# Optimization experiments

Measured on AMD Instinct MI355X. Metric: run time of the kernel, lower is better.

The kernel has to match this reference:

```python
import jax, jax.numpy as jnp
import numpy as np

HEADS = 16
EMBED = 1024


def setup_inputs() -> dict:
    key = jax.random.key(0)
    k1, k2, k3, k4, k5, k6 = jax.random.split(key, 6)
    N, S, E = 2, 2048, EMBED
    return {
        "values": jax.random.normal(k1, (N, S, E), dtype=jnp.float32),
        "keys": jax.random.normal(k2, (N, S, E), dtype=jnp.float32),
        "query": jax.random.normal(k3, (N, S, E), dtype=jnp.float32),
        "mask": jax.random.randint(k4, (N, 1, S, S), 0, 2, dtype=jnp.int32),
        "W_out": jax.random.normal(k5, (E, E), dtype=jnp.float32) * 0.02,
        "b_out": jax.random.normal(k6, (E,), dtype=jnp.float32) * 0.02,
    }


def reference(values, keys, query, mask, W_out, b_out):
    N, Q, E = query.shape
    K = keys.shape[1]
    H = HEADS
    D = E // H
    v = values.reshape(N, K, H, D)
    k = keys.reshape(N, K, H, D)
    q = query.reshape(N, Q, H, D)
    # [N, H, Q, K] score matrix (faithful to the naive einsum formulation)
    energy = jnp.einsum("nqhd,nkhd->nhqk", q, k)
    energy = jnp.where(mask == 0, jnp.float32(-1e20), energy)
    # NOTE: original scales by sqrt(embed_size), not sqrt(head_dim)
    attention = jax.nn.softmax(energy / jnp.sqrt(jnp.float32(E)), axis=3)
    out = jnp.einsum("nhqk,nkhd->nqhd", attention, v).reshape(N, Q, E)
    return out @ W_out.T + b_out
```

## Files before the change

kernel.cpp:

```cpp
#include <hip/hip_runtime.h>
#include <hip/hip_bf16.h>


#define S_LEN  2048
#define EMB    1024
#define NHEAD  16
#define DHEAD  64
#define NBATCH 2

#define KSC 0.04508422002778011f

typedef float              f32x4    __attribute__((ext_vector_type(4)));
typedef float              f32x16   __attribute__((ext_vector_type(16)));
typedef __bf16             bf16x8   __attribute__((ext_vector_type(8)));
typedef unsigned short     ushort8v __attribute__((ext_vector_type(8)));
typedef unsigned long long u64;

union FragU { ushort8v u; bf16x8 b; };
union BFrag { unsigned u32[4]; bf16x8 b; };

__device__ __forceinline__ unsigned short f2b(float f) {
  union { __hip_bfloat16 h; unsigned short u; } c;
  c.h = __float2bfloat16(f);
  return c.u;
}

__device__ __forceinline__ unsigned int cvt_pk_bf16(float lo, float hi) {
  unsigned int r;
  asm("v_cvt_pk_bf16_f32 %0, %1, %2" : "=v"(r) : "v"(lo), "v"(hi));
  return r;
}

#define PSWAP(a, b) asm("v_permlane32_swap_b32 %0, %1" : "+v"(a), "+v"(b))

#define GLD16(g, l)                                                            \
  __builtin_amdgcn_global_load_lds(                                            \
      (__attribute__((address_space(1))) void*)(g),                            \
      (__attribute__((address_space(3))) void*)(l), 16, 0, 0)

__global__ __launch_bounds__(256) void prep(
    const float* __restrict__ Wo, unsigned short* __restrict__ Wb,
    const float* __restrict__ Kg, unsigned short* __restrict__ Kb,
    const float* __restrict__ Vg, unsigned short* __restrict__ Vt,
    const int* __restrict__ Mg,   u64* __restrict__ Mb)
{
  const int bid = blockIdx.x;
  const int tid = threadIdx.x;
  if (bid < 2560) {
    const float* X = (bid < 512) ? Wo : Kg;
    unsigned short* Y = (bid < 512) ? Wb : Kb;
    const int bb = (bid < 512) ? bid : bid - 512;
    const size_t i = ((size_t)bb * 256 + tid) * 8;
    float4 a = *reinterpret_cast<const float4*>(X + i);
    float4 b = *reinterpret_cast<const float4*>(X + i + 4);
    ushort8v u;
    u[0] = f2b(a.x); u[1] = f2b(a.y); u[2] = f2b(a.z); u[3] = f2b(a.w);
    u[4] = f2b(b.x); u[5] = f2b(b.y); u[6] = f2b(b.z); u[7] = f2b(b.w);
    *reinterpret_cast<ushort8v*>(Y + i) = u;
  } else if (bid < 3584) {
    __shared__ unsigned short T[64][72];
    const int b2 = bid - 2560;
    const int sb = b2 & 31, h = (b2 >> 5) & 15, n = b2 >> 9;
    const int r = tid >> 2, cb = (tid & 3) * 16;
    const float* src = Vg + ((size_t)(n * S_LEN + sb * 64 + r)) * EMB + h * DHEAD + cb;
    ushort8v u0, u1;
#pragma unroll
    for (int j = 0; j < 2; ++j) {
      float4 x = *reinterpret_cast<const float4*>(src + j * 4);
      u0[j*4+0] = f2b(x.x); u0[j*4+1] = f2b(x.y); u0[j*4+2] = f2b(x.z); u0[j*4+3] = f2b(x.w);
      float4 y = *reinterpret_cast<const float4*>(src + 8 + j * 4);
      u1[j*4+0] = f2b(y.x); u1[j*4+1] = f2b(y.y); u1[j*4+2] = f2b(y.z); u1[j*4+3] = f2b(y.w);
    }
    *reinterpret_cast<ushort8v*>(&T[r][cb])     = u0;
    *reinterpret_cast<ushort8v*>(&T[r][cb + 8]) = u1;
    __syncthreads();
    const int d = tid >> 2, sc_ = (tid & 3) * 16;
    ushort8v o0, o1;
#pragma unroll
    for (int j = 0; j < 8; ++j) { o0[j] = T[sc_ + j][d]; o1[j] = T[sc_ + 8 + j][d]; }
    unsigned short* dst = Vt + ((size_t)((n * NHEAD + h) * DHEAD + d)) * S_LEN + sb * 64 + sc_;
    *reinterpret_cast<ushort8v*>(dst)     = o0;
    *reinterpret_cast<ushort8v*>(dst + 8) = o1;
  } else {
    const int b3 = bid - 3584;
    const size_t base = (size_t)b3 * 1024 + (tid >> 6) * 256;
    const int l = tid & 63;
#pragma unroll
    for (int j = 0; j < 4; ++j) {
      const int v = Mg[base + j * 64 + l];
      u64 bj = __ballot(v != 0);
      if (l == 0) Mb[base / 64 + j] = bj;
    }
  }
}

__global__ __launch_bounds__(512, 4) void attn_fwd(
    const unsigned short* __restrict__ Kb,
    const unsigned short* __restrict__ Vtg,
    const float* __restrict__ Qg,
    const u64* __restrict__ Mbit,
    unsigned short* __restrict__ Og)
{
  __shared__ __attribute__((aligned(16))) char SMEM[65536];

  const int bid = blockIdx.x;
  const int qb = bid & 15, h = (bid >> 4) & 15, n = bid >> 8;
  const int nh = n * NHEAD + h;
  const int tid = threadIdx.x;
  const int w = tid >> 6, sp = w >> 2, wq = w & 3;
  const int l = tid & 63, q5 = l & 31, hi = l >> 5;
  const int hi4 = hi * 4;
  const int q0w = qb * 128 + wq * 32;
  const int qg = q0w + q5;

  FragU qf[4];
  {
    const float* qp = Qg + ((size_t)(n * S_LEN + qg)) * EMB + h * DHEAD + hi * 8;
#pragma unroll
    for (int s = 0; s < 4; ++s) {
      float4 a = *reinterpret_cast<const float4*>(qp + s * 16);
      float4 b = *reinterpret_cast<const float4*>(qp + s * 16 + 4);
      ushort8v u;
      u[0] = f2b(a.x * KSC); u[1] = f2b(a.y * KSC); u[2] = f2b(a.z * KSC); u[3] = f2b(a.w * KSC);
      u[4] = f2b(b.x * KSC); u[5] = f2b(b.y * KSC); u[6] = f2b(b.z * KSC); u[7] = f2b(b.w * KSC);
      qf[s].u = u;
    }
  }

  FragU ones;
#pragma unroll
  for (int j = 0; j < 8; ++j) ones.u[j] = 0x3F80;

  f32x16 acc0 = {}, acc1 = {}, racc = {};

  const int t8 = tid & 255;
  const int srow = t8 >> 3, sc = t8 & 7;
  const char* kbase = (const char*)Kb +
      ((size_t)(n * S_LEN + sp * 1024 + srow)) * 2048 + h * 128 +
      ((sc * 16) ^ ((srow & 7) << 4));
  const char* vbase = (const char*)Vtg +
      ((size_t)(nh * DHEAD + srow)) * 4096 + sp * 2048 +
      ((sc * 16) ^ ((srow & 7) << 4));

  char* Ksp = SMEM + sp * 16384;
  char* Vsp = SMEM + 32768 + sp * 16384;
  const int fsw = (l & 7) << 4;

  const u64* Mq = Mbit + ((size_t)(n * S_LEN + qg)) * 32 + sp * 16;
  u64 mq_cur = Mq[0];

#define ATTN_STAGE(BUF, IT) do {                                               \
    GLD16(kbase + (size_t)(IT) * 131072,          Ksp + (BUF) * 8192 + t8 * 16); \
    GLD16(kbase + (size_t)(IT) * 131072 + 65536,  Ksp + (BUF) * 8192 + 4096 + t8 * 16); \
    GLD16(vbase + (size_t)(IT) * 128,             Vsp + (BUF) * 8192 + t8 * 16); \
    GLD16(vbase + (size_t)(IT) * 128 + 131072,    Vsp + (BUF) * 8192 + 4096 + t8 * 16); \
  } while (0)

#define ATTN_TILE(BUF, IT) do {                                                \
    __syncthreads();                                                           \
    if ((IT) + 1 < 16) ATTN_STAGE((BUF) ^ 1, (IT) + 1);                        \
    const u64 mrow_ = mq_cur;                                                  \
    if ((IT) + 1 < 16) mq_cur = Mq[(IT) + 1];                                  \
    _Pragma("unroll") for (int b = 0; b < 2; ++b) {                            \
      f32x16 Sb = {};                                                          \
      __builtin_amdgcn_s_setprio(1);                                           \
      _Pragma("unroll") for (int s = 0; s < 4; ++s) {                          \
        FragU kf_;                                                             \
        kf_.u = *reinterpret_cast<const ushort8v*>(                            \
            Ksp + (BUF) * 8192 + ((b * 32 + q5) * 128 + ((s * 32 + hi * 16) ^ fsw))); \
        Sb = __builtin_amdgcn_mfma_f32_32x32x16_bf16(kf_.b, qf[s].b, Sb, 0, 0, 0); \
      }                                                                        \
      __builtin_amdgcn_s_setprio(0);                                           \
      const unsigned m32_ = b ? (unsigned)(mrow_ >> 32) : (unsigned)mrow_;     \
      float p_[16];                                                            \
      _Pragma("unroll") for (int t = 0; t < 4; ++t) {                          \
        const unsigned nib_ = m32_ >> (8 * t + hi4);                           \
        _Pragma("unroll") for (int e = 0; e < 4; ++e) {                        \
          const int r = 4 * t + e;                                             \
          float ex_ = __builtin_amdgcn_exp2f(Sb[r]);                           \
          const unsigned sm_ = (unsigned)((int)(nib_ << (31 - e)) >> 31);      \
          p_[r] = __uint_as_float(__float_as_uint(ex_) & sm_);                 \
        }                                                                      \
      }                                                                        \
      unsigned U0 = cvt_pk_bf16(p_[0],  p_[1]),  U1 = cvt_pk_bf16(p_[2],  p_[3]); \
      unsigned U2 = cvt_pk_bf16(p_[4],  p_[5]),  U3 = cvt_pk_bf16(p_[6],  p_[7]); \
      unsigned U4 = cvt_pk_bf16(p_[8],  p_[9]),  U5 = cvt_pk_bf16(p_[10], p_[11]); \
      unsigned U6 = cvt_pk_bf16(p_[12], p_[13]), U7 = cvt_pk_bf16(p_[14], p_[15]); \
      PSWAP(U0, U2); PSWAP(U1, U3); PSWAP(U4, U6); PSWAP(U5, U7);              \
      BFrag F0, F1;                                                            \
      F0.u32[0] = U0; F0.u32[1] = U1; F0.u32[2] = U2; F0.u32[3] = U3;          \
      F1.u32[0] = U4; F1.u32[1] = U5; F1.u32[2] = U6; F1.u32[3] = U7;          \
      __builtin_amdgcn_s_setprio(1);                                           \
      racc = __builtin_amdgcn_mfma_f32_32x32x16_bf16(ones.b, F0.b, racc, 0, 0, 0); \
      racc = __builtin_amdgcn_mfma_f32_32x32x16_bf16(ones.b, F1.b, racc, 0, 0, 0); \
      _Pragma("unroll") for (int db = 0; db < 2; ++db) {                       \
        FragU vf0_, vf1_;                                                      \
        vf0_.u = *reinterpret_cast<const ushort8v*>(                           \
            Vsp + (BUF) * 8192 + ((db * 32 + q5) * 128 + (((2 * b) * 32 + hi * 16) ^ fsw))); \
        vf1_.u = *reinterpret_cast<const ushort8v*>(                           \
            Vsp + (BUF) * 8192 + ((db * 32 + q5) * 128 + (((2 * b + 1) * 32 + hi * 16) ^ fsw))); \
        if (db == 0) {                                                         \
          acc0 = __builtin_amdgcn_mfma_f32_32x32x16_bf16(vf0_.b, F0.b, acc0, 0, 0, 0); \
          acc0 = __builtin_amdgcn_mfma_f32_32x32x16_bf16(vf1_.b, F1.b, acc0, 0, 0, 0); \
        } else {                                                               \
          acc1 = __builtin_amdgcn_mfma_f32_32x32x16_bf16(vf0_.b, F0.b, acc1, 0, 0, 0); \
          acc1 = __builtin_amdgcn_mfma_f32_32x32x16_bf16(vf1_.b, F1.b, acc1, 0, 0, 0); \
        }                                                                      \
      }                                                                        \
      __builtin_amdgcn_s_setprio(0);                                           \
    }                                                                          \
  } while (0)

  ATTN_STAGE(0, 0);
  for (int it = 0; it < 16; it += 2) {
    ATTN_TILE(0, it);
    ATTN_TILE(1, it + 1);
  }

  const float rs = racc[0];
  const int esw = (l & 7) << 4;

  __syncthreads();
  if (sp == 1) {
#pragma unroll
    for (int i = 0; i < 4; ++i) {
      f32x4 v0 = (f32x4){acc0[4*i], acc0[4*i+1], acc0[4*i+2], acc0[4*i+3]};
      f32x4 v1 = (f32x4){acc1[4*i], acc1[4*i+1], acc1[4*i+2], acc1[4*i+3]};
      *reinterpret_cast<f32x4*>(SMEM + wq * 8192 + l * 128 + ((i * 16) ^ esw))      = v0;
      *reinterpret_cast<f32x4*>(SMEM + wq * 8192 + l * 128 + ((64 + i * 16) ^ esw)) = v1;
    }
    *reinterpret_cast<float*>(SMEM + 32768 + wq * 256 + l * 4) = rs;
  }
  __syncthreads();
  if (sp == 0) {
    const float ors = *reinterpret_cast<const float*>(SMEM + 32768 + wq * 256 + l * 4);
    const float rin = 1.0f / (rs + ors);
    unsigned short* orow = Og + ((size_t)(n * S_LEN + qg)) * EMB + h * DHEAD + hi4;
#pragma unroll
    for (int db = 0; db < 2; ++db) {
#pragma unroll
      for (int t = 0; t < 4; ++t) {
        f32x4 pa = *reinterpret_cast<const f32x4*>(
            SMEM + wq * 8192 + l * 128 + ((db * 64 + t * 16) ^ esw));
        float a0, a1, a2, a3;
        if (db == 0) {
          a0 = (acc0[4*t]   + pa[0]) * rin; a1 = (acc0[4*t+1] + pa[1]) * rin;
          a2 = (acc0[4*t+2] + pa[2]) * rin; a3 = (acc0[4*t+3] + pa[3]) * rin;
        } else {
          a0 = (acc1[4*t]   + pa[0]) * rin; a1 = (acc1[4*t+1] + pa[1]) * rin;
          a2 = (acc1[4*t+2] + pa[2]) * rin; a3 = (acc1[4*t+3] + pa[3]) * rin;
        }
        uint2 pk;
        pk.x = cvt_pk_bf16(a0, a1);
        pk.y = cvt_pk_bf16(a2, a3);
        *reinterpret_cast<uint2*>(orow + db * 32 + t * 8) = pk;
      }
    }
  }
}

__global__ __launch_bounds__(256) void out_proj(
    const unsigned short* __restrict__ A,
    const unsigned short* __restrict__ W,
    const float* __restrict__ bias,
    float* __restrict__ Y)
{
  __shared__ __attribute__((aligned(16))) unsigned short At[2][8192];
  __shared__ __attribute__((aligned(16))) unsigned short Bt[2][4096];

  const int bid = blockIdx.x;
  const int nb = bid & 15, mb = bid >> 4;
  const int tid = threadIdx.x;
  const int w = tid >> 6, l = tid & 63, lg = l >> 4, li = l & 15;
  const int m0 = mb * 128, n0 = nb * 64;

  f32x4 acc[2][4];
#pragma unroll
  for (int g = 0; g < 2; ++g)
#pragma unroll
    for (int c = 0; c < 4; ++c) acc[g][c] = (f32x4){0.f, 0.f, 0.f, 0.f};

  const int srow8  = tid >> 3;
  const int schunk = (tid & 7) * 16;
  const int ssw    = (srow8 & 7) << 4;
  const char* abase = (const char*)A + ((size_t)m0 + srow8) * (EMB * 2) + (schunk ^ ssw);
  const char* bbase = (const char*)W + ((size_t)n0 + srow8) * (EMB * 2) + (schunk ^ ssw);
  const int rsw = (li & 7) << 4;

#define PROJ_STAGE(BUF, KK) do {                                               \
    const char* ab_ = abase + (KK) * 128;                                      \
    const char* bb_ = bbase + (KK) * 128;                                      \
    GLD16(ab_,             (char*)At + (BUF) * 16384 + w * 1024);              \
    GLD16(ab_ + 32 * 2048, (char*)At + (BUF) * 16384 + 4096 + w * 1024);       \
    GLD16(ab_ + 64 * 2048, (char*)At + (BUF) * 16384 + 8192 + w * 1024);       \
    GLD16(ab_ + 96 * 2048, (char*)At + (BUF) * 16384 + 12288 + w * 1024);      \
    GLD16(bb_,             (char*)Bt + (BUF) * 8192 + w * 1024);               \
    GLD16(bb_ + 32 * 2048, (char*)Bt + (BUF) * 8192 + 4096 + w * 1024);        \
  } while (0)

#define PROJ_TILE(BUF, KK) do {                                                \
    __syncthreads();                                                           \
    if ((KK) + 1 < 16) PROJ_STAGE((BUF) ^ 1, (KK) + 1);                        \
    __builtin_amdgcn_s_setprio(1);                                             \
    _Pragma("unroll") for (int s = 0; s < 2; ++s) {                            \
      FragU af_[2];                                                            \
      _Pragma("unroll") for (int g = 0; g < 2; ++g)                            \
        af_[g].u = *reinterpret_cast<const ushort8v*>(                         \
            (char*)At + (BUF) * 16384 +                                        \
            ((w * 32 + g * 16 + li) * 128 + ((s * 64 + lg * 16) ^ rsw)));      \
      _Pragma("unroll") for (int c = 0; c < 4; ++c) {                          \
        FragU bf_;                                                             \
        bf_.u = *reinterpret_cast<const ushort8v*>(                            \
            (char*)Bt + (BUF) * 8192 +                                         \
            ((c * 16 + li) * 128 + ((s * 64 + lg * 16) ^ rsw)));               \
        acc[0][c] = __builtin_amdgcn_mfma_f32_16x16x32_bf16(af_[0].b, bf_.b, acc[0][c], 0, 0, 0); \
        acc[1][c] = __builtin_amdgcn_mfma_f32_16x16x32_bf16(af_[1].b, bf_.b, acc[1][c], 0, 0, 0); \
      }                                                                        \
    }                                                                          \
    __builtin_amdgcn_s_setprio(0);                                             \
  } while (0)

  PROJ_STAGE(0, 0);
  for (int kk = 0; kk < 16; kk += 2) {
    PROJ_TILE(0, kk);
    PROJ_TILE(1, kk + 1);
  }

#pragma unroll
  for (int g = 0; g < 2; ++g)
#pragma unroll
    for (int c = 0; c < 4; ++c) {
      const float bv = bias[n0 + c * 16 + li];
#pragma unroll
      for (int r = 0; r < 4; ++r) {
        const int row = m0 + w * 32 + g * 16 + lg * 4 + r;
        Y[(size_t)row * EMB + n0 + c * 16 + li] = acc[g][c][r] + bv;
      }
    }
}

extern "C" void kernel_launch(void* const* d_in, const int* in_sizes, int n_in,
                              void* d_out, int out_size, void* d_ws, size_t ws_size,
                              hipStream_t stream) {
  const float* Vg = (const float*)d_in[0];
  const float* Kg = (const float*)d_in[1];
  const float* Qg = (const float*)d_in[2];
  const int*   Mg = (const int*)d_in[3];
  const float* Wo = (const float*)d_in[4];
  const float* bo = (const float*)d_in[5];
  float* Y = (float*)d_out;

  char* ws = (char*)d_ws;
  unsigned short* Og   = (unsigned short*)(ws);
  unsigned short* Wb   = (unsigned short*)(ws + (8u << 20));
  unsigned short* Kb16 = (unsigned short*)(ws + (10u << 20));
  unsigned short* Vt   = (unsigned short*)(ws + (18u << 20));
  u64*            Mbit = (u64*)(ws + (26u << 20));

  hipLaunchKernelGGL(prep, dim3(11776), dim3(256), 0, stream,
                     Wo, Wb, Kg, Kb16, Vg, Vt, Mg, Mbit);
  hipLaunchKernelGGL(attn_fwd, dim3(NBATCH * NHEAD * (S_LEN / 128)), dim3(512), 0, stream,
                     Kb16, Vt, Qg, Mbit, Og);
  hipLaunchKernelGGL(out_proj, dim3((NBATCH * S_LEN / 128) * (EMB / 64)), dim3(256), 0, stream,
                     Og, Wb, bo, Y);
}
```

Before: 88.92 us.

## Drop LDS staging in attention, load K/V fragments directly from global memory

The attention kernel drops its LDS double-buffered K/V staging and the two-way key split with its cross-warp reduction. Each of four warps now reads K and V fragments straight from global memory (relying on L2) for all 32 key tiles. Q is pre-converted to scaled bf16 in the prep kernel, and blocks are remapped so neighbouring blocks share heads. This removes barriers and LDS traffic but adds redundant global loads per warp, exposes load latency with no explicit prefetch, and cuts threads per block.

```diff
diff --git a/kernel.cpp b/kernel.cpp
--- a/kernel.cpp
+++ b/kernel.cpp
@@ -41,25 +41,27 @@
 __global__ __launch_bounds__(256) void prep(
     const float* __restrict__ Wo, unsigned short* __restrict__ Wb,
     const float* __restrict__ Kg, unsigned short* __restrict__ Kb,
+    const float* __restrict__ Qg, unsigned short* __restrict__ Qb,
     const float* __restrict__ Vg, unsigned short* __restrict__ Vt,
     const int* __restrict__ Mg,   u64* __restrict__ Mb)
 {
   const int bid = blockIdx.x;
   const int tid = threadIdx.x;
-  if (bid < 2560) {
-    const float* X = (bid < 512) ? Wo : Kg;
-    unsigned short* Y = (bid < 512) ? Wb : Kb;
-    const int bb = (bid < 512) ? bid : bid - 512;
+  if (bid < 4608) {
+    const float* X; unsigned short* Y; int bb; float scl;
+    if (bid < 512)       { X = Wo; Y = Wb; bb = bid;        scl = 1.f; }
+    else if (bid < 2560) { X = Kg; Y = Kb; bb = bid - 512;  scl = 1.f; }
+    else                 { X = Qg; Y = Qb; bb = bid - 2560; scl = KSC; }
     const size_t i = ((size_t)bb * 256 + tid) * 8;
     float4 a = *reinterpret_cast<const float4*>(X + i);
     float4 b = *reinterpret_cast<const float4*>(X + i + 4);
     ushort8v u;
-    u[0] = f2b(a.x); u[1] = f2b(a.y); u[2] = f2b(a.z); u[3] = f2b(a.w);
-    u[4] = f2b(b.x); u[5] = f2b(b.y); u[6] = f2b(b.z); u[7] = f2b(b.w);
+    u[0] = f2b(a.x * scl); u[1] = f2b(a.y * scl); u[2] = f2b(a.z * scl); u[3] = f2b(a.w * scl);
+    u[4] = f2b(b.x * scl); u[5] = f2b(b.y * scl); u[6] = f2b(b.z * scl); u[7] = f2b(b.w * scl);
     *reinterpret_cast<ushort8v*>(Y + i) = u;
-  } else if (bid < 3584) {
+  } else if (bid < 5632) {
     __shared__ unsigned short T[64][72];
-    const int b2 = bid - 2560;
+    const int b2 = bid - 4608;
     const int sb = b2 & 31, h = (b2 >> 5) & 15, n = b2 >> 9;
     const int r = tid >> 2, cb = (tid & 3) * 16;
     const float* src = Vg + ((size_t)(n * S_LEN + sb * 64 + r)) * EMB + h * DHEAD + cb;
@@ -82,7 +84,7 @@
     *reinterpret_cast<ushort8v*>(dst)     = o0;
     *reinterpret_cast<ushort8v*>(dst + 8) = o1;
   } else {
-    const int b3 = bid - 3584;
+    const int b3 = bid - 5632;
     const size_t base = (size_t)b3 * 1024 + (tid >> 6) * 256;
     const int l = tid & 63;
 #pragma unroll
@@ -94,37 +96,29 @@
   }
 }
 
-__global__ __launch_bounds__(512, 4) void attn_fwd(
+__global__ __launch_bounds__(256, 4) void attn_fwd(
     const unsigned short* __restrict__ Kb,
     const unsigned short* __restrict__ Vtg,
-    const float* __restrict__ Qg,
+    const unsigned short* __restrict__ Qb,
     const u64* __restrict__ Mbit,
     unsigned short* __restrict__ Og)
 {
-  __shared__ __attribute__((aligned(16))) char SMEM[65536];
-
-  const int bid = blockIdx.x;
-  const int qb = bid & 15, h = (bid >> 4) & 15, n = bid >> 8;
+  const int bid0 = blockIdx.x;
+  const int ob = ((bid0 & 7) << 6) | (bid0 >> 3);
+  const int qb = ob & 15, h = (ob >> 4) & 15, n = ob >> 8;
   const int nh = n * NHEAD + h;
   const int tid = threadIdx.x;
-  const int w = tid >> 6, sp = w >> 2, wq = w & 3;
+  const int w = tid >> 6;
   const int l = tid & 63, q5 = l & 31, hi = l >> 5;
   const int hi4 = hi * 4;
-  const int q0w = qb * 128 + wq * 32;
-  const int qg = q0w + q5;
+  const int qg = qb * 128 + w * 32 + q5;
 
   FragU qf[4];
   {
-    const float* qp = Qg + ((size_t)(n * S_LEN + qg)) * EMB + h * DHEAD + hi * 8;
-#pragma unroll
-    for (int s = 0; s < 4; ++s) {
-      float4 a = *reinterpret_cast<const float4*>(qp + s * 16);
-      float4 b = *reinterpret_cast<const float4*>(qp + s * 16 + 4);
-      ushort8v u;
-      u[0] = f2b(a.x * KSC); u[1] = f2b(a.y * KSC); u[2] = f2b(a.z * KSC); u[3] = f2b(a.w * KSC);
-      u[4] = f2b(b.x * KSC); u[5] = f2b(b.y * KSC); u[6] = f2b(b.z * KSC); u[7] = f2b(b.w * KSC);
-      qf[s].u = u;
-    }
+    const unsigned short* qp = Qb + ((size_t)(n * S_LEN + qg)) * EMB + h * DHEAD + hi * 8;
+#pragma unroll
+    for (int s = 0; s < 4; ++s)
+      qf[s].u = *reinterpret_cast<const ushort8v*>(qp + s * 16);
   }
 
   FragU ones;
@@ -133,128 +127,81 @@
 
   f32x16 acc0 = {}, acc1 = {}, racc = {};
 
-  const int t8 = tid & 255;
-  const int srow = t8 >> 3, sc = t8 & 7;
-  const char* kbase = (const char*)Kb +
-      ((size_t)(n * S_LEN + sp * 1024 + srow)) * 2048 + h * 128 +
-      ((sc * 16) ^ ((srow & 7) << 4));
-  const char* vbase = (const char*)Vtg +
-      ((size_t)(nh * DHEAD + srow)) * 4096 + sp * 2048 +
-      ((sc * 16) ^ ((srow & 7) << 4));
-
-  char* Ksp = SMEM + sp * 16384;
-  char* Vsp = SMEM + 32768 + sp * 16384;
-  const int fsw = (l & 7) << 4;
-
-  const u64* Mq = Mbit + ((size_t)(n * S_LEN + qg)) * 32 + sp * 16;
-  u64 mq_cur = Mq[0];
-
-#define ATTN_STAGE(BUF, IT) do {                                               \
-    GLD16(kbase + (size_t)(IT) * 131072,          Ksp + (BUF) * 8192 + t8 * 16); \
-    GLD16(kbase + (size_t)(IT) * 131072 + 65536,  Ksp + (BUF) * 8192 + 4096 + t8 * 16); \
-    GLD16(vbase + (size_t)(IT) * 128,             Vsp + (BUF) * 8192 + t8 * 16); \
-    GLD16(vbase + (size_t)(IT) * 128 + 131072,    Vsp + (BUF) * 8192 + 4096 + t8 * 16); \
-  } while (0)
-
-#define ATTN_TILE(BUF, IT) do {                                                \
-    __syncthreads();                                                           \
-    if ((IT) + 1 < 16) ATTN_STAGE((BUF) ^ 1, (IT) + 1);                        \
-    const u64 mrow_ = mq_cur;                                                  \
-    if ((IT) + 1 < 16) mq_cur = Mq[(IT) + 1];                                  \
-    _Pragma("unroll") for (int b = 0; b < 2; ++b) {                            \
-      f32x16 Sb = {};                                                          \
-      __builtin_amdgcn_s_setprio(1);                                           \
-      _Pragma("unroll") for (int s = 0; s < 4; ++s) {                          \
-        FragU kf_;                                                             \
-        kf_.u = *reinterpret_cast<const ushort8v*>(                            \
-            Ksp + (BUF) * 8192 + ((b * 32 + q5) * 128 + ((s * 32 + hi * 16) ^ fsw))); \
-        Sb = __builtin_amdgcn_mfma_f32_32x32x16_bf16(kf_.b, qf[s].b, Sb, 0, 0, 0); \
-      }                                                                        \
-      __builtin_amdgcn_s_setprio(0);                                           \
-      const unsigned m32_ = b ? (unsigned)(mrow_ >> 32) : (unsigned)mrow_;     \
-      float p_[16];                                                            \
-      _Pragma("unroll") for (int t = 0; t < 4; ++t) {                          \
-        const unsigned nib_ = m32_ >> (8 * t + hi4);                           \
-        _Pragma("unroll") for (int e = 0; e < 4; ++e) {                        \
-          const int r = 4 * t + e;                                             \
-          float ex_ = __builtin_amdgcn_exp2f(Sb[r]);                           \
-          const unsigned sm_ = (unsigned)((int)(nib_ << (31 - e)) >> 31);      \
-          p_[r] = __uint_as_float(__float_as_uint(ex_) & sm_);                 \
-        }                                                                      \
-      }                                                                        \
-      unsigned U0 = cvt_pk_bf16(p_[0],  p_[1]),  U1 = cvt_pk_bf16(p_[2],  p_[3]); \
-      unsigned U2 = cvt_pk_bf16(p_[4],  p_[5]),  U3 = cvt_pk_bf16(p_[6],  p_[7]); \
-      unsigned U4 = cvt_pk_bf16(p_[8],  p_[9]),  U5 = cvt_pk_bf16(p_[10], p_[11]); \
-      unsigned U6 = cvt_pk_bf16(p_[12], p_[13]), U7 = cvt_pk_bf16(p_[14], p_[15]); \
-      PSWAP(U0, U2); PSWAP(U1, U3); PSWAP(U4, U6); PSWAP(U5, U7);              \
-      BFrag F0, F1;                                                            \
-      F0.u32[0] = U0; F0.u32[1] = U1; F0.u32[2] = U2; F0.u32[3] = U3;          \
-      F1.u32[0] = U4; F1.u32[1] = U5; F1.u32[2] = U6; F1.u32[3] = U7;          \
-      __builtin_amdgcn_s_setprio(1);                                           \
-      racc = __builtin_amdgcn_mfma_f32_32x32x16_bf16(ones.b, F0.b, racc, 0, 0, 0); \
-      racc = __builtin_amdgcn_mfma_f32_32x32x16_bf16(ones.b, F1.b, racc, 0, 0, 0); \
-      _Pragma("unroll") for (int db = 0; db < 2; ++db) {                       \
-        FragU vf0_, vf1_;                                                      \
-        vf0_.u = *reinterpret_cast<const ushort8v*>(                           \
-            Vsp + (BUF) * 8192 + ((db * 32 + q5) * 128 + (((2 * b) * 32 + hi * 16) ^ fsw))); \
-        vf1_.u = *reinterpret_cast<const ushort8v*>(                           \
-            Vsp + (BUF) * 8192 + ((db * 32 + q5) * 128 + (((2 * b + 1) * 32 + hi * 16) ^ fsw))); \
-        if (db == 0) {                                                         \
-          acc0 = __builtin_amdgcn_mfma_f32_32x32x16_bf16(vf0_.b, F0.b, acc0, 0, 0, 0); \
-          acc0 = __builtin_amdgcn_mfma_f32_32x32x16_bf16(vf1_.b, F1.b, acc0, 0, 0, 0); \
-        } else {                                                               \
-          acc1 = __builtin_amdgcn_mfma_f32_32x32x16_bf16(vf0_.b, F0.b, acc1, 0, 0, 0); \
-          acc1 = __builtin_amdgcn_mfma_f32_32x32x16_bf16(vf1_.b, F1.b, acc1, 0, 0, 0); \
-        }                                                                      \
-      }                                                                        \
-      __builtin_amdgcn_s_setprio(0);                                           \
-    }                                                                          \
-  } while (0)
-
-  ATTN_STAGE(0, 0);
-  for (int it = 0; it < 16; it += 2) {
-    ATTN_TILE(0, it);
-    ATTN_TILE(1, it + 1);
-  }
-
-  const float rs = racc[0];
-  const int esw = (l & 7) << 4;
-
-  __syncthreads();
-  if (sp == 1) {
-#pragma unroll
-    for (int i = 0; i < 4; ++i) {
-      f32x4 v0 = (f32x4){acc0[4*i], acc0[4*i+1], acc0[4*i+2], acc0[4*i+3]};
-      f32x4 v1 = (f32x4){acc1[4*i], acc1[4*i+1], acc1[4*i+2], acc1[4*i+3]};
-      *reinterpret_cast<f32x4*>(SMEM + wq * 8192 + l * 128 + ((i * 16) ^ esw))      = v0;
-      *reinterpret_cast<f32x4*>(SMEM + wq * 8192 + l * 128 + ((64 + i * 16) ^ esw)) = v1;
-    }
-    *reinterpret_cast<float*>(SMEM + 32768 + wq * 256 + l * 4) = rs;
-  }
-  __syncthreads();
-  if (sp == 0) {
-    const float ors = *reinterpret_cast<const float*>(SMEM + 32768 + wq * 256 + l * 4);
-    const float rin = 1.0f / (rs + ors);
-    unsigned short* orow = Og + ((size_t)(n * S_LEN + qg)) * EMB + h * DHEAD + hi4;
-#pragma unroll
-    for (int db = 0; db < 2; ++db) {
+  const char* kbl = (const char*)Kb + ((size_t)(n * S_LEN) + q5) * 2048 + h * 128 + hi * 16;
+  const char* vbl = (const char*)Vtg + ((size_t)(nh * DHEAD) + q5) * 4096 + hi * 16;
+  const u64* Mq = Mbit + ((size_t)(n * S_LEN) + qg) * 32;
+
+#pragma unroll 2
+  for (int it = 0; it < 32; ++it) {
+    const u64 mrow = Mq[it];
+    const char* kt = kbl + (size_t)it * 131072;
+    const char* vt = vbl + (size_t)it * 128;
+#pragma unroll
+    for (int b = 0; b < 2; ++b) {
+      f32x16 Sb = {};
+#pragma unroll
+      for (int s = 0; s < 4; ++s) {
+        FragU kf;
+        kf.u = *reinterpret_cast<const ushort8v*>(kt + b * 65536 + s * 32);
+        Sb = __builtin_amdgcn_mfma_f32_32x32x16_bf16(kf.b, qf[s].b, Sb, 0, 0, 0);
+      }
+      const unsigned m32_ = b ? (unsigned)(mrow >> 32) : (unsigned)mrow;
+      float p_[16];
 #pragma unroll
       for (int t = 0; t < 4; ++t) {
-        f32x4 pa = *reinterpret_cast<const f32x4*>(
-            SMEM + wq * 8192 + l * 128 + ((db * 64 + t * 16) ^ esw));
-        float a0, a1, a2, a3;
+        const unsigned nib_ = m32_ >> (8 * t + hi4);
+#pragma unroll
+        for (int e = 0; e < 4; ++e) {
+          const int r = 4 * t + e;
+          float ex_ = __builtin_amdgcn_exp2f(Sb[r]);
+          const unsigned sm_ = (unsigned)((int)(nib_ << (31 - e)) >> 31);
+          p_[r] = __uint_as_float(__float_as_uint(ex_) & sm_);
+        }
+      }
+      unsigned U0 = cvt_pk_bf16(p_[0],  p_[1]),  U1 = cvt_pk_bf16(p_[2],  p_[3]);
+      unsigned U2 = cvt_pk_bf16(p_[4],  p_[5]),  U3 = cvt_pk_bf16(p_[6],  p_[7]);
+      unsigned U4 = cvt_pk_bf16(p_[8],  p_[9]),  U5 = cvt_pk_bf16(p_[10], p_[11]);
+      unsigned U6 = cvt_pk_bf16(p_[12], p_[13]), U7 = cvt_pk_bf16(p_[14], p_[15]);
+      PSWAP(U0, U2); PSWAP(U1, U3); PSWAP(U4, U6); PSWAP(U5, U7);
+      BFrag F0, F1;
+      F0.u32[0] = U0; F0.u32[1] = U1; F0.u32[2] = U2; F0.u32[3] = U3;
+      F1.u32[0] = U4; F1.u32[1] = U5; F1.u32[2] = U6; F1.u32[3] = U7;
+      racc = __builtin_amdgcn_mfma_f32_32x32x16_bf16(ones.b, F0.b, racc, 0, 0, 0);
+      racc = __builtin_amdgcn_mfma_f32_32x32x16_bf16(ones.b, F1.b, racc, 0, 0, 0);
+#pragma unroll
+      for (int db = 0; db < 2; ++db) {
+        FragU vf0, vf1;
+        vf0.u = *reinterpret_cast<const ushort8v*>(vt + db * 131072 + (2 * b) * 32);
+        vf1.u = *reinterpret_cast<const ushort8v*>(vt + db * 131072 + (2 * b + 1) * 32);
         if (db == 0) {
-          a0 = (acc0[4*t]   + pa[0]) * rin; a1 = (acc0[4*t+1] + pa[1]) * rin;
-          a2 = (acc0[4*t+2] + pa[2]) * rin; a3 = (acc0[4*t+3] + pa[3]) * rin;
+          acc0 = __builtin_amdgcn_mfma_f32_32x32x16_bf16(vf0.b, F0.b, acc0, 0, 0, 0);
+          acc0 = __builtin_amdgcn_mfma_f32_32x32x16_bf16(vf1.b, F1.b, acc0, 0, 0, 0);
         } else {
-          a0 = (acc1[4*t]   + pa[0]) * rin; a1 = (acc1[4*t+1] + pa[1]) * rin;
-          a2 = (acc1[4*t+2] + pa[2]) * rin; a3 = (acc1[4*t+3] + pa[3]) * rin;
+          acc1 = __builtin_amdgcn_mfma_f32_32x32x16_bf16(vf0.b, F0.b, acc1, 0, 0, 0);
+          acc1 = __builtin_amdgcn_mfma_f32_32x32x16_bf16(vf1.b, F1.b, acc1, 0, 0, 0);
         }
-        uint2 pk;
-        pk.x = cvt_pk_bf16(a0, a1);
-        pk.y = cvt_pk_bf16(a2, a3);
-        *reinterpret_cast<uint2*>(orow + db * 32 + t * 8) = pk;
-      }
+      }
+    }
+  }
+
+  const float rin = 1.0f / racc[0];
+  unsigned short* orow = Og + ((size_t)(n * S_LEN + qg)) * EMB + h * DHEAD + hi4;
+#pragma unroll
+  for (int db = 0; db < 2; ++db) {
+#pragma unroll
+    for (int t = 0; t < 4; ++t) {
+      float a0, a1, a2, a3;
+      if (db == 0) {
+        a0 = acc0[4*t] * rin;   a1 = acc0[4*t+1] * rin;
+        a2 = acc0[4*t+2] * rin; a3 = acc0[4*t+3] * rin;
+      } else {
+        a0 = acc1[4*t] * rin;   a1 = acc1[4*t+1] * rin;
+        a2 = acc1[4*t+2] * rin; a3 = acc1[4*t+3] * rin;
+      }
+      uint2 pk;
+      pk.x = cvt_pk_bf16(a0, a1);
+      pk.y = cvt_pk_bf16(a2, a3);
+      *reinterpret_cast<uint2*>(orow + db * 32 + t * 8) = pk;
     }
   }
 }
@@ -356,11 +303,12 @@
   unsigned short* Kb16 = (unsigned short*)(ws + (10u << 20));
   unsigned short* Vt   = (unsigned short*)(ws + (18u << 20));
   u64*            Mbit = (u64*)(ws + (26u << 20));
-
-  hipLaunchKernelGGL(prep, dim3(11776), dim3(256), 0, stream,
-                     Wo, Wb, Kg, Kb16, Vg, Vt, Mg, Mbit);
-  hipLaunchKernelGGL(attn_fwd, dim3(NBATCH * NHEAD * (S_LEN / 128)), dim3(512), 0, stream,
-                     Kb16, Vt, Qg, Mbit, Og);
+  unsigned short* Qb16 = (unsigned short*)(ws + (27u << 20));
+
+  hipLaunchKernelGGL(prep, dim3(13824), dim3(256), 0, stream,
+                     Wo, Wb, Kg, Kb16, Qg, Qb16, Vg, Vt, Mg, Mbit);
+  hipLaunchKernelGGL(attn_fwd, dim3(NBATCH * NHEAD * (S_LEN / 128)), dim3(256), 0, stream,
+                     Kb16, Vt, Qb16, Mbit, Og);
   hipLaunchKernelGGL(out_proj, dim3((NBATCH * S_LEN / 128) * (EMB / 64)), dim3(256), 0, stream,
                      Og, Wb, bo, Y);
 }
```

Result: slower. 170.8 us (+92.1%).

## Enlarge out_proj tile to 128x128 with 2x2 warp layout

Applied to the files above, without the earlier changes.

The output projection GEMM now uses 128x128 output tiles instead of 128x64. Each of the four waves computes a 64x64 subtile with 4x4 MFMA accumulators, which raises operand reuse from LDS and halves the number of workgroups to 256. LDS staging is merged into one 64KB buffer, setprio hints are removed, and launch bounds request two blocks per CU. The cost is higher register pressure and fewer blocks to fill the GPU, which leaves some CUs idle on a 256-CU device.

```diff
diff --git a/kernel.cpp b/kernel.cpp
--- a/kernel.cpp
+++ b/kernel.cpp
@@ -259,65 +259,64 @@
   }
 }
 
-__global__ __launch_bounds__(256) void out_proj(
+__global__ __launch_bounds__(256, 2) void out_proj(
     const unsigned short* __restrict__ A,
     const unsigned short* __restrict__ W,
     const float* __restrict__ bias,
     float* __restrict__ Y)
 {
-  __shared__ __attribute__((aligned(16))) unsigned short At[2][8192];
-  __shared__ __attribute__((aligned(16))) unsigned short Bt[2][4096];
+  __shared__ __attribute__((aligned(16))) char PSM[65536];
 
   const int bid = blockIdx.x;
-  const int nb = bid & 15, mb = bid >> 4;
+  const int nb = bid & 7, mb = bid >> 3;
   const int tid = threadIdx.x;
-  const int w = tid >> 6, l = tid & 63, lg = l >> 4, li = l & 15;
-  const int m0 = mb * 128, n0 = nb * 64;
-
-  f32x4 acc[2][4];
-#pragma unroll
-  for (int g = 0; g < 2; ++g)
-#pragma unroll
-    for (int c = 0; c < 4; ++c) acc[g][c] = (f32x4){0.f, 0.f, 0.f, 0.f};
-
-  const int srow8  = tid >> 3;
-  const int schunk = (tid & 7) * 16;
-  const int ssw    = (srow8 & 7) << 4;
-  const char* abase = (const char*)A + ((size_t)m0 + srow8) * (EMB * 2) + (schunk ^ ssw);
-  const char* bbase = (const char*)W + ((size_t)n0 + srow8) * (EMB * 2) + (schunk ^ ssw);
+  const int w = tid >> 6, wr = w >> 1, wc = w & 1;
+  const int l = tid & 63, lg = l >> 4, li = l & 15;
+  const int m0 = mb * 128, n0 = nb * 128;
+
+  f32x4 acc[4][4];
+#pragma unroll
+  for (int mi = 0; mi < 4; ++mi)
+#pragma unroll
+    for (int ci = 0; ci < 4; ++ci) acc[mi][ci] = (f32x4){0.f, 0.f, 0.f, 0.f};
+
+  const int srow = tid >> 3;
+  const int sch  = (tid & 7) * 16;
+  const int ssw  = (srow & 7) << 4;
+  const char* abase = (const char*)A + ((size_t)(m0 + srow)) * 2048 + (sch ^ ssw);
+  const char* bbase = (const char*)W + ((size_t)(n0 + srow)) * 2048 + (sch ^ ssw);
   const int rsw = (li & 7) << 4;
 
+  char* Asm = PSM;
+  char* Bsm = PSM + 32768;
+
 #define PROJ_STAGE(BUF, KK) do {                                               \
-    const char* ab_ = abase + (KK) * 128;                                      \
-    const char* bb_ = bbase + (KK) * 128;                                      \
-    GLD16(ab_,             (char*)At + (BUF) * 16384 + w * 1024);              \
-    GLD16(ab_ + 32 * 2048, (char*)At + (BUF) * 16384 + 4096 + w * 1024);       \
-    GLD16(ab_ + 64 * 2048, (char*)At + (BUF) * 16384 + 8192 + w * 1024);       \
-    GLD16(ab_ + 96 * 2048, (char*)At + (BUF) * 16384 + 12288 + w * 1024);      \
-    GLD16(bb_,             (char*)Bt + (BUF) * 8192 + w * 1024);               \
-    GLD16(bb_ + 32 * 2048, (char*)Bt + (BUF) * 8192 + 4096 + w * 1024);        \
+    _Pragma("unroll") for (int j = 0; j < 4; ++j) {                            \
+      GLD16(abase + (size_t)j * 65536 + (KK) * 128,                            \
+            Asm + (BUF) * 16384 + j * 4096 + tid * 16);                        \
+      GLD16(bbase + (size_t)j * 65536 + (KK) * 128,                            \
+            Bsm + (BUF) * 16384 + j * 4096 + tid * 16);                        \
+    }                                                                          \
   } while (0)
 
 #define PROJ_TILE(BUF, KK) do {                                                \
     __syncthreads();                                                           \
     if ((KK) + 1 < 16) PROJ_STAGE((BUF) ^ 1, (KK) + 1);                        \
-    __builtin_amdgcn_s_setprio(1);                                             \
     _Pragma("unroll") for (int s = 0; s < 2; ++s) {                            \
-      FragU af_[2];                                                            \
-      _Pragma("unroll") for (int g = 0; g < 2; ++g)                            \
-        af_[g].u = *reinterpret_cast<const ushort8v*>(                         \
-            (char*)At + (BUF) * 16384 +                                        \
-            ((w * 32 + g * 16 + li) * 128 + ((s * 64 + lg * 16) ^ rsw)));      \
-      _Pragma("unroll") for (int c = 0; c < 4; ++c) {                          \
-        FragU bf_;                                                             \
-        bf_.u = *reinterpret_cast<const ushort8v*>(                            \
-            (char*)Bt + (BUF) * 8192 +                                         \
-            ((c * 16 + li) * 128 + ((s * 64 + lg * 16) ^ rsw)));               \
-        acc[0][c] = __builtin_amdgcn_mfma_f32_16x16x32_bf16(af_[0].b, bf_.b, acc[0][c], 0, 0, 0); \
-        acc[1][c] = __builtin_amdgcn_mfma_f32_16x16x32_bf16(af_[1].b, bf_.b, acc[1][c], 0, 0, 0); \
-      }                                                                        \
+      FragU af_[4], bf_[4];                                                    \
+      _Pragma("unroll") for (int mi = 0; mi < 4; ++mi)                         \
+        af_[mi].u = *reinterpret_cast<const ushort8v*>(                        \
+            Asm + (BUF) * 16384 +                                              \
+            ((wr * 64 + mi * 16 + li) * 128 + ((s * 64 + lg * 16) ^ rsw)));    \
+      _Pragma("unroll") for (int ci = 0; ci < 4; ++ci)                         \
+        bf_[ci].u = *reinterpret_cast<const ushort8v*>(                        \
+            Bsm + (BUF) * 16384 +                                              \
+            ((wc * 64 + ci * 16 + li) * 128 + ((s * 64 + lg * 16) ^ rsw)));    \
+      _Pragma("unroll") for (int mi = 0; mi < 4; ++mi)                         \
+        _Pragma("unroll") for (int ci = 0; ci < 4; ++ci)                       \
+          acc[mi][ci] = __builtin_amdgcn_mfma_f32_16x16x32_bf16(               \
+              af_[mi].b, bf_[ci].b, acc[mi][ci], 0, 0, 0);                     \
     }                                                                          \
-    __builtin_amdgcn_s_setprio(0);                                             \
   } while (0)
 
   PROJ_STAGE(0, 0);
@@ -327,16 +326,18 @@
   }
 
 #pragma unroll
-  for (int g = 0; g < 2; ++g)
-#pragma unroll
-    for (int c = 0; c < 4; ++c) {
-      const float bv = bias[n0 + c * 16 + li];
+  for (int ci = 0; ci < 4; ++ci) {
+    const int col = n0 + wc * 64 + ci * 16 + li;
+    const float bv = bias[col];
+#pragma unroll
+    for (int mi = 0; mi < 4; ++mi) {
 #pragma unroll
       for (int r = 0; r < 4; ++r) {
-        const int row = m0 + w * 32 + g * 16 + lg * 4 + r;
-        Y[(size_t)row * EMB + n0 + c * 16 + li] = acc[g][c][r] + bv;
+        const int row = m0 + wr * 64 + mi * 16 + lg * 4 + r;
+        Y[(size_t)row * EMB + col] = acc[mi][ci][r] + bv;
       }
     }
+  }
 }
 
 extern "C" void kernel_launch(void* const* d_in, const int* in_sizes, int n_in,
@@ -361,6 +362,6 @@
                      Wo, Wb, Kg, Kb16, Vg, Vt, Mg, Mbit);
   hipLaunchKernelGGL(attn_fwd, dim3(NBATCH * NHEAD * (S_LEN / 128)), dim3(512), 0, stream,
                      Kb16, Vt, Qg, Mbit, Og);
-  hipLaunchKernelGGL(out_proj, dim3((NBATCH * S_LEN / 128) * (EMB / 64)), dim3(256), 0, stream,
+  hipLaunchKernelGGL(out_proj, dim3((NBATCH * S_LEN / 128) * (EMB / 128)), dim3(256), 0, stream,
                      Og, Wb, bo, Y);
 }
```

After: 87.27 us (median of 2 runs). No clear change (-1.9%).
